# Optimization experiments

Hardware: AMD Instinct MI355X
Metric: run time of the kernel (lower is better)

The kernel has to match this reference:

```python
import jax, jax.numpy as jnp
import numpy as np

F_FEAT = 310   # len(feature_names)
B = 2048       # samples; x has F_FEAT*B elements
H = 32         # sfp_neurons


def _uniform(key, shape, bound):
    return jax.random.uniform(key, shape, jnp.float32, -bound, bound)


def setup_inputs() -> dict:
    key = jax.random.key(0)
    ks = jax.random.split(key, 7)
    x = jax.random.normal(ks[0], (F_FEAT, B), dtype=jnp.float32)
    # Stacked per-feature MLP params (torch Linear default init: U(-1/sqrt(fan_in), +)).
    s1 = 1.0 / np.sqrt(F_FEAT - 1)
    s2 = 1.0 / np.sqrt(H)
    W1 = _uniform(ks[1], (F_FEAT, F_FEAT - 1, H), s1)  # (in, out) layout
    b1 = _uniform(ks[2], (F_FEAT, H), s1)
    W2 = _uniform(ks[3], (F_FEAT, H, H), s2)
    b2 = _uniform(ks[4], (F_FEAT, H), s2)
    W3 = _uniform(ks[5], (F_FEAT, H, H), s2)
    b3 = _uniform(ks[6], (F_FEAT, H), s2)
    return {"x": x, "W1": W1, "b1": b1, "W2": W2, "b2": b2, "W3": W3, "b3": b3}


def reference(x, W1, b1, W2, b2, W3, b3):
    F_, B_ = x.shape
    # Leave-one-out gather: for SFP i, rows [0..i-1, i+1..F-1] of x (feature-major),
    # then the original's view(-1, 1, F-1) reinterprets the flat buffer as (B, F-1).
    idx = jnp.arange(F_ - 1)[None, :]
    idx = idx + (idx >= jnp.arange(F_)[:, None])          # (F, F-1)
    X = x[idx].reshape(F_, B_, F_ - 1)                    # (F, B, F-1) grouped inputs
    h = jax.nn.relu(jnp.einsum('fbk,fkh->fbh', X, W1) + b1[:, None, :])
    h = jax.nn.relu(jnp.einsum('fbh,fhg->fbg', h, W2) + b2[:, None, :])
    h = jax.nn.relu(jnp.einsum('fbh,fhg->fbg', h, W3) + b3[:, None, :])  # (F, B, H)
    # torch.cat of per-SFP .view(-1) == row-major flatten of (F, B, H)
    return h.reshape(-1)
```

## Files before the change

### kernel.cpp

```cpp
#include <hip/hip_runtime.h>

namespace {

constexpr int F_FEAT = 310;
constexpr int KDIM   = 309;
constexpr int BSZ    = 2048;
constexpr int HDIM   = 32;
constexpr int NCH    = 10;
constexpr int NX     = F_FEAT * BSZ;

constexpr int    NBLK8   = NX / 8 + 2;
constexpr size_t CSTR_B  = (size_t)NBLK8 * 16;
constexpr size_t XC_BYTES = CSTR_B * 8;
constexpr size_t W1T_FSTR = 32 * 640;
constexpr size_t W1T_OFF  = XC_BYTES;
constexpr size_t W2T_OFF  = W1T_OFF + (size_t)F_FEAT * W1T_FSTR;
constexpr size_t WT_FSTR  = 2048;
constexpr size_t W3T_OFF  = W2T_OFF + (size_t)F_FEAT * WT_FSTR;
constexpr size_t WS_NEED  = W3T_OFF + (size_t)F_FEAT * WT_FSTR;

typedef __bf16 bf16x8 __attribute__((ext_vector_type(8)));
typedef __bf16 bf16x4 __attribute__((ext_vector_type(4)));
typedef float  f32x4  __attribute__((ext_vector_type(4)));

#define MFMA(a, b, c) __builtin_amdgcn_mfma_f32_16x16x32_bf16((a), (b), (c), 0, 0, 0)

__global__ __launch_bounds__(256) void cvt_x(const float* __restrict__ x,
                                             char* __restrict__ ws) {
    const int m = blockIdx.x * 256 + threadIdx.x;
    const int c = blockIdx.y;
    if (m >= NBLK8) return;
    const int e0 = m * 8 - c;
    bf16x8 v;
    #pragma unroll
    for (int q = 0; q < 8; ++q) {
        const int i = e0 + q;
        const float f = (i >= 0 && i < NX) ? x[i] : 0.f;
        v[q] = (__bf16)f;
    }
    *(bf16x8*)(ws + (size_t)c * CSTR_B + (size_t)m * 16) = v;
}

__global__ __launch_bounds__(256) void cvt_w(const float* __restrict__ W1,
                                             const float* __restrict__ W2,
                                             const float* __restrict__ W3,
                                             char* __restrict__ ws) {
    __shared__ float tile[32][33];
    const int fi = blockIdx.x, tid = threadIdx.x;
    const int kl = tid >> 3;
    const int h4 = (tid & 7) * 4;

    {
        const float* Wg = W1 + (size_t)fi * KDIM * HDIM;
        char* wt = ws + W1T_OFF + (size_t)fi * W1T_FSTR;
        for (int kc = 0; kc < NCH; ++kc) {
            const int k = kc * 32 + kl;
            float4 f = (k < KDIM) ? *(const float4*)&Wg[k * HDIM + h4]
                                  : make_float4(0.f, 0.f, 0.f, 0.f);
            tile[kl][h4 + 0] = f.x; tile[kl][h4 + 1] = f.y;
            tile[kl][h4 + 2] = f.z; tile[kl][h4 + 3] = f.w;
            __syncthreads();
            const int h = kl, kq = h4;
            bf16x4 o;
            #pragma unroll
            for (int j = 0; j < 4; ++j) o[j] = (__bf16)tile[kq + j][h];
            const int boff = (h * 640 + 2 * (kc * 32 + kq)) ^ ((h & 7) << 4);
            *(bf16x4*)(wt + boff) = o;
            __syncthreads();
        }
    }
    {
        const float* Wg = W2 + (size_t)fi * HDIM * HDIM;
        char* wt = ws + W2T_OFF + (size_t)fi * WT_FSTR;
        float4 f = *(const float4*)&Wg[kl * HDIM + h4];
        tile[kl][h4 + 0] = f.x; tile[kl][h4 + 1] = f.y;
        tile[kl][h4 + 2] = f.z; tile[kl][h4 + 3] = f.w;
        __syncthreads();
        bf16x4 o;
        #pragma unroll
        for (int j = 0; j < 4; ++j) o[j] = (__bf16)tile[h4 + j][kl];
        *(bf16x4*)(wt + (kl * 32 + h4) * 2) = o;
        __syncthreads();
    }
    {
        const float* Wg = W3 + (size_t)fi * HDIM * HDIM;
        char* wt = ws + W3T_OFF + (size_t)fi * WT_FSTR;
        float4 f = *(const float4*)&Wg[kl * HDIM + h4];
        tile[kl][h4 + 0] = f.x; tile[kl][h4 + 1] = f.y;
        tile[kl][h4 + 2] = f.z; tile[kl][h4 + 3] = f.w;
        __syncthreads();
        bf16x4 o;
        #pragma unroll
        for (int j = 0; j < 4; ++j) o[j] = (__bf16)tile[h4 + j][kl];
        *(bf16x4*)(wt + (kl * 32 + h4) * 2) = o;
    }
}

template<bool FAST>
__global__ __launch_bounds__(256) void sfp2(
    const float* __restrict__ x,
    const float* __restrict__ W1, const float* __restrict__ b1,
    const float* __restrict__ W2, const float* __restrict__ b2,
    const float* __restrict__ W3, const float* __restrict__ b3,
    const char* __restrict__ ws, float* __restrict__ out)
{
    __shared__ __attribute__((aligned(16))) __bf16 W1s[32 * 320];
    __shared__ __attribute__((aligned(16))) __bf16 h1s[128 * 40];

    int fi, sb;
    if (FAST) {
        const int xc = blockIdx.x & 7, li = blockIdx.x >> 3;
        const int cnt = (xc < 6) ? 39 : 38;
        const int lf = li >> 4;
        if (lf >= cnt) return;
        fi = ((xc < 6) ? xc * 39 : 234 + (xc - 6) * 38) + lf;
        sb = li & 15;
    } else {
        fi = blockIdx.x >> 4; sb = blockIdx.x & 15;
    }

    const int tid = threadIdx.x, lane = tid & 63, wv = tid >> 6;
    const int l15 = lane & 15, l16 = lane >> 4;
    const int lk8 = l16 * 8, r0 = l16 * 4;
    const int b0 = sb << 7, iB = fi << 11;

    if (FAST) {
        const char* src = ws + W1T_OFF + (size_t)fi * W1T_FSTR;
        #pragma unroll
        for (int i = 0; i < 5; ++i) {
            const int off = i * 4096 + tid * 16;
            *(bf16x8*)((char*)W1s + off) = *(const bf16x8*)(src + off);
        }
        __syncthreads();
    }

    const float b1v0 = b1[fi*HDIM + l15], b1v1 = b1[fi*HDIM + 16 + l15];
    const float b2v0 = b2[fi*HDIM + l15], b2v1 = b2[fi*HDIM + 16 + l15];
    const float b3v0 = b3[fi*HDIM + l15], b3v1 = b3[fi*HDIM + 16 + l15];

    auto loadA = [&](int lin) -> bf16x8 {
        if (FAST) {
            if ((unsigned)(iB - 1 - lin) < 7u) {
                bf16x8 r;
                #pragma unroll
                for (int q = 0; q < 8; ++q) {
                    int i = lin + q; i += (i >= iB) ? BSZ : 0;
                    r[q] = *(const __bf16*)(ws + (size_t)i * 2);
                }
                return r;
            }
            const int e  = lin + ((lin >= iB) ? BSZ : 0);
            const int c8 = (-e) & 7;
            return *(const bf16x8*)(ws + (size_t)c8 * CSTR_B + (size_t)(e + c8) * 2);
        } else {
            bf16x8 r;
            #pragma unroll
            for (int q = 0; q < 8; ++q) {
                int i = lin + q; i += (i >= iB) ? BSZ : 0;
                i = (i < NX) ? i : (NX - 1);
                r[q] = (__bf16)x[i];
            }
            return r;
        }
    };

    auto loadW1f = [&](int c, int hrow) -> bf16x8 {
        if (FAST) {
            const int boff = (hrow * 640 + 2 * (c * 32 + lk8)) ^ ((hrow & 7) << 4);
            return *(const bf16x8*)((const char*)W1s + boff);
        } else {
            const float* Wg = W1 + (size_t)fi * KDIM * HDIM;
            bf16x8 r;
            #pragma unroll
            for (int q = 0; q < 8; ++q) {
                const int k = c * 32 + lk8 + q;
                r[q] = (__bf16)((k < KDIM) ? Wg[k * HDIM + hrow] : 0.f);
            }
            return r;
        }
    };

    f32x4 acc00 = {0,0,0,0}, acc01 = {0,0,0,0}, acc10 = {0,0,0,0}, acc11 = {0,0,0,0};
    const int mrow = wv * 32;
    const int lin0 = (b0 + mrow + l15) * KDIM + lk8;
    const int lin1 = lin0 + 16 * KDIM;

    bf16x8 a0 = loadA(lin0),        a1 = loadA(lin1);
    bf16x8 w0 = loadW1f(0, l15),    w1 = loadW1f(0, 16 + l15);
    for (int c = 0; c < NCH; ++c) {
        bf16x8 na0, na1, nw0, nw1;
        if (c + 1 < NCH) {
            na0 = loadA(lin0 + 32 * (c + 1));
            na1 = loadA(lin1 + 32 * (c + 1));
            nw0 = loadW1f(c + 1, l15);
            nw1 = loadW1f(c + 1, 16 + l15);
        }
        acc00 = MFMA(a0, w0, acc00);
        acc01 = MFMA(a0, w1, acc01);
        acc10 = MFMA(a1, w0, acc10);
        acc11 = MFMA(a1, w1, acc11);
        a0 = na0; a1 = na1; w0 = nw0; w1 = nw1;
    }

    constexpr int LDA = 40;
    #pragma unroll
    for (int r = 0; r < 4; ++r) {
        float v;
        v = acc00[r] + b1v0; h1s[(mrow +      r0 + r)*LDA +      l15] = (__bf16)(v > 0.f ? v : 0.f);
        v = acc01[r] + b1v1; h1s[(mrow +      r0 + r)*LDA + 16 + l15] = (__bf16)(v > 0.f ? v : 0.f);
        v = acc10[r] + b1v0; h1s[(mrow + 16 + r0 + r)*LDA +      l15] = (__bf16)(v > 0.f ? v : 0.f);
        v = acc11[r] + b1v1; h1s[(mrow + 16 + r0 + r)*LDA + 16 + l15] = (__bf16)(v > 0.f ? v : 0.f);
    }

    auto loadW23 = [&](const float* Wg, size_t toff, int hrow) -> bf16x8 {
        if (FAST) {
            return *(const bf16x8*)(ws + toff + (size_t)fi * WT_FSTR
                                    + (size_t)(hrow * 32 + lk8) * 2);
        } else {
            bf16x8 r;
            #pragma unroll
            for (int q = 0; q < 8; ++q)
                r[q] = (__bf16)Wg[(size_t)fi * HDIM * HDIM + (lk8 + q) * HDIM + hrow];
            return r;
        }
    };

    const f32x4 z = {0,0,0,0};
    f32x4 c200, c201, c210, c211;
    {
        bf16x8 ha0 = *(const bf16x8*)&h1s[(mrow +      l15)*LDA + lk8];
        bf16x8 ha1 = *(const bf16x8*)&h1s[(mrow + 16 + l15)*LDA + lk8];
        bf16x8 v0 = loadW23(W2, W2T_OFF, l15);
        bf16x8 v1 = loadW23(W2, W2T_OFF, 16 + l15);
        c200 = MFMA(ha0, v0, z); c201 = MFMA(ha0, v1, z);
        c210 = MFMA(ha1, v0, z); c211 = MFMA(ha1, v1, z);
    }
    #pragma unroll
    for (int r = 0; r < 4; ++r) {
        float v;
        v = c200[r] + b2v0; h1s[(mrow +      r0 + r)*LDA +      l15] = (__bf16)(v > 0.f ? v : 0.f);
        v = c201[r] + b2v1; h1s[(mrow +      r0 + r)*LDA + 16 + l15] = (__bf16)(v > 0.f ? v : 0.f);
        v = c210[r] + b2v0; h1s[(mrow + 16 + r0 + r)*LDA +      l15] = (__bf16)(v > 0.f ? v : 0.f);
        v = c211[r] + b2v1; h1s[(mrow + 16 + r0 + r)*LDA + 16 + l15] = (__bf16)(v > 0.f ? v : 0.f);
    }

    f32x4 c300, c301, c310, c311;
    {
        bf16x8 ha0 = *(const bf16x8*)&h1s[(mrow +      l15)*LDA + lk8];
        bf16x8 ha1 = *(const bf16x8*)&h1s[(mrow + 16 + l15)*LDA + lk8];
        bf16x8 v0 = loadW23(W3, W3T_OFF, l15);
        bf16x8 v1 = loadW23(W3, W3T_OFF, 16 + l15);
        c300 = MFMA(ha0, v0, z); c301 = MFMA(ha0, v1, z);
        c310 = MFMA(ha1, v0, z); c311 = MFMA(ha1, v1, z);
    }

    const size_t orow = (size_t)(fi * BSZ + b0 + mrow);
    #pragma unroll
    for (int r = 0; r < 4; ++r) {
        float v;
        v = c300[r] + b3v0; out[(orow +      r0 + r)*HDIM +      l15] = v > 0.f ? v : 0.f;
        v = c301[r] + b3v1; out[(orow +      r0 + r)*HDIM + 16 + l15] = v > 0.f ? v : 0.f;
        v = c310[r] + b3v0; out[(orow + 16 + r0 + r)*HDIM +      l15] = v > 0.f ? v : 0.f;
        v = c311[r] + b3v1; out[(orow + 16 + r0 + r)*HDIM + 16 + l15] = v > 0.f ? v : 0.f;
    }
}

}

extern "C" void kernel_launch(void* const* d_in, const int* in_sizes, int n_in,
                              void* d_out, int out_size, void* d_ws, size_t ws_size,
                              hipStream_t stream) {
    const float* x  = (const float*)d_in[0];
    const float* W1 = (const float*)d_in[1];
    const float* b1 = (const float*)d_in[2];
    const float* W2 = (const float*)d_in[3];
    const float* b2 = (const float*)d_in[4];
    const float* W3 = (const float*)d_in[5];
    const float* b3 = (const float*)d_in[6];
    float* out = (float*)d_out;
    char* ws = (char*)d_ws;

    const bool fast = (ws != nullptr) && (ws_size >= WS_NEED);
    if (fast) {
        hipLaunchKernelGGL(cvt_x, dim3((NBLK8 + 255) / 256, 8), dim3(256), 0, stream, x, ws);
        hipLaunchKernelGGL(cvt_w, dim3(F_FEAT), dim3(256), 0, stream, W1, W2, W3, ws);
        hipLaunchKernelGGL((sfp2<true>), dim3(8 * 39 * 16), dim3(256), 0, stream,
                           x, W1, b1, W2, b2, W3, b3, ws, out);
    } else {
        hipLaunchKernelGGL((sfp2<false>), dim3(F_FEAT * 16), dim3(256), 0, stream,
                           x, W1, b1, W2, b2, W3, b3, ws, out);
    }
}
```

Measured before the change: 77.91 us.

## Merge conversion kernels and read W1 directly from global memory

Result: slower. 99.86 us (+28.2%).

```diff
diff --git a/kernel.cpp b/kernel.cpp
--- a/kernel.cpp
+++ b/kernel.cpp
@@ -9,102 +9,113 @@
 constexpr int NCH    = 10;
 constexpr int NX     = F_FEAT * BSZ;
 
-constexpr int    NBLK8   = NX / 8 + 2;
-constexpr size_t CSTR_B  = (size_t)NBLK8 * 16;
+constexpr int    NBLK8    = NX / 8 + 2;
+constexpr size_t CSTR_B   = (size_t)NBLK8 * 16;
 constexpr size_t XC_BYTES = CSTR_B * 8;
-constexpr size_t W1T_FSTR = 32 * 640;
+constexpr size_t W1T_FSTR = 32 * 320 * 2;
 constexpr size_t W1T_OFF  = XC_BYTES;
 constexpr size_t W2T_OFF  = W1T_OFF + (size_t)F_FEAT * W1T_FSTR;
-constexpr size_t WT_FSTR  = 2048;
+constexpr size_t WT_FSTR  = 32 * 32 * 2;
 constexpr size_t W3T_OFF  = W2T_OFF + (size_t)F_FEAT * WT_FSTR;
 constexpr size_t WS_NEED  = W3T_OFF + (size_t)F_FEAT * WT_FSTR;
 
+constexpr int NBX      = (NBLK8 + 255) / 256;
+constexpr int CVT_XBLK = NBX * 8;
+constexpr int CVT_BLK  = CVT_XBLK + F_FEAT * 6;
+
 typedef __bf16 bf16x8 __attribute__((ext_vector_type(8)));
-typedef __bf16 bf16x4 __attribute__((ext_vector_type(4)));
 typedef float  f32x4  __attribute__((ext_vector_type(4)));
 
 #define MFMA(a, b, c) __builtin_amdgcn_mfma_f32_16x16x32_bf16((a), (b), (c), 0, 0, 0)
 
-__global__ __launch_bounds__(256) void cvt_x(const float* __restrict__ x,
-                                             char* __restrict__ ws) {
-    const int m = blockIdx.x * 256 + threadIdx.x;
-    const int c = blockIdx.y;
-    if (m >= NBLK8) return;
-    const int e0 = m * 8 - c;
-    bf16x8 v;
-    #pragma unroll
-    for (int q = 0; q < 8; ++q) {
-        const int i = e0 + q;
-        const float f = (i >= 0 && i < NX) ? x[i] : 0.f;
-        v[q] = (__bf16)f;
-    }
-    *(bf16x8*)(ws + (size_t)c * CSTR_B + (size_t)m * 16) = v;
-}
-
-__global__ __launch_bounds__(256) void cvt_w(const float* __restrict__ W1,
-                                             const float* __restrict__ W2,
-                                             const float* __restrict__ W3,
-                                             char* __restrict__ ws) {
-    __shared__ float tile[32][33];
-    const int fi = blockIdx.x, tid = threadIdx.x;
-    const int kl = tid >> 3;
-    const int h4 = (tid & 7) * 4;
-
-    {
+__global__ __launch_bounds__(256) void cvt_all(
+    const float* __restrict__ x,  const float* __restrict__ W1,
+    const float* __restrict__ W2, const float* __restrict__ W3,
+    char* __restrict__ ws)
+{
+    __shared__ float tile[64][33];
+    const int b = blockIdx.x, tid = threadIdx.x;
+
+    if (b < CVT_XBLK) {
+        const int c = b / NBX, mb = b - c * NBX;
+        const int m = mb * 256 + tid;
+        if (m >= NBLK8) return;
+        const int e0 = m * 8 - c;
+        bf16x8 v;
+        #pragma unroll
+        for (int q = 0; q < 8; ++q) {
+            const int i = e0 + q;
+            v[q] = (__bf16)((i >= 0 && i < NX) ? x[i] : 0.f);
+        }
+        *(bf16x8*)(ws + (size_t)c * CSTR_B + (size_t)m * 16) = v;
+        return;
+    }
+
+    const int wb = b - CVT_XBLK;
+    const int fi = wb / 6, part = wb - fi * 6;
+
+    if (part < 5) {
         const float* Wg = W1 + (size_t)fi * KDIM * HDIM;
-        char* wt = ws + W1T_OFF + (size_t)fi * W1T_FSTR;
-        for (int kc = 0; kc < NCH; ++kc) {
-            const int k = kc * 32 + kl;
-            float4 f = (k < KDIM) ? *(const float4*)&Wg[k * HDIM + h4]
-                                  : make_float4(0.f, 0.f, 0.f, 0.f);
-            tile[kl][h4 + 0] = f.x; tile[kl][h4 + 1] = f.y;
-            tile[kl][h4 + 2] = f.z; tile[kl][h4 + 3] = f.w;
+        const int row = tid >> 2;
+        const int c8  = (tid & 3) * 8;
+        const int k   = part * 64 + row;
+        float4 f0 = make_float4(0,0,0,0), f1 = f0;
+        if (k < KDIM) {
+            f0 = *(const float4*)&Wg[k * HDIM + c8];
+            f1 = *(const float4*)&Wg[k * HDIM + c8 + 4];
+        }
+        tile[row][c8+0] = f0.x; tile[row][c8+1] = f0.y;
+        tile[row][c8+2] = f0.z; tile[row][c8+3] = f0.w;
+        tile[row][c8+4] = f1.x; tile[row][c8+5] = f1.y;
+        tile[row][c8+6] = f1.z; tile[row][c8+7] = f1.w;
+        __syncthreads();
+        const int h = tid & 31, kq = (tid >> 5) * 8;
+        bf16x8 o;
+        #pragma unroll
+        for (int j = 0; j < 8; ++j) o[j] = (__bf16)tile[kq + j][h];
+        *(bf16x8*)(ws + W1T_OFF + (size_t)fi * W1T_FSTR
+                   + (size_t)(h * 320 + part * 64 + kq) * 2) = o;
+    } else {
+        const int kl = tid >> 3, h4 = (tid & 7) * 4;
+        const int h = tid & 31, kq = (tid >> 5) * 8;
+        {
+            const float* Wg = W2 + (size_t)fi * HDIM * HDIM;
+            float4 f = *(const float4*)&Wg[kl * HDIM + h4];
+            tile[kl][h4+0] = f.x; tile[kl][h4+1] = f.y;
+            tile[kl][h4+2] = f.z; tile[kl][h4+3] = f.w;
             __syncthreads();
-            const int h = kl, kq = h4;
-            bf16x4 o;
-            #pragma unroll
-            for (int j = 0; j < 4; ++j) o[j] = (__bf16)tile[kq + j][h];
-            const int boff = (h * 640 + 2 * (kc * 32 + kq)) ^ ((h & 7) << 4);
-            *(bf16x4*)(wt + boff) = o;
+            if (tid < 128) {
+                bf16x8 o;
+                #pragma unroll
+                for (int j = 0; j < 8; ++j) o[j] = (__bf16)tile[kq + j][h];
+                *(bf16x8*)(ws + W2T_OFF + (size_t)fi * WT_FSTR + (size_t)(h * 32 + kq) * 2) = o;
+            }
             __syncthreads();
         }
-    }
-    {
-        const float* Wg = W2 + (size_t)fi * HDIM * HDIM;
-        char* wt = ws + W2T_OFF + (size_t)fi * WT_FSTR;
-        float4 f = *(const float4*)&Wg[kl * HDIM + h4];
-        tile[kl][h4 + 0] = f.x; tile[kl][h4 + 1] = f.y;
-        tile[kl][h4 + 2] = f.z; tile[kl][h4 + 3] = f.w;
-        __syncthreads();
-        bf16x4 o;
-        #pragma unroll
-        for (int j = 0; j < 4; ++j) o[j] = (__bf16)tile[h4 + j][kl];
-        *(bf16x4*)(wt + (kl * 32 + h4) * 2) = o;
-        __syncthreads();
-    }
-    {
-        const float* Wg = W3 + (size_t)fi * HDIM * HDIM;
-        char* wt = ws + W3T_OFF + (size_t)fi * WT_FSTR;
-        float4 f = *(const float4*)&Wg[kl * HDIM + h4];
-        tile[kl][h4 + 0] = f.x; tile[kl][h4 + 1] = f.y;
-        tile[kl][h4 + 2] = f.z; tile[kl][h4 + 3] = f.w;
-        __syncthreads();
-        bf16x4 o;
-        #pragma unroll
-        for (int j = 0; j < 4; ++j) o[j] = (__bf16)tile[h4 + j][kl];
-        *(bf16x4*)(wt + (kl * 32 + h4) * 2) = o;
+        {
+            const float* Wg = W3 + (size_t)fi * HDIM * HDIM;
+            float4 f = *(const float4*)&Wg[kl * HDIM + h4];
+            tile[kl][h4+0] = f.x; tile[kl][h4+1] = f.y;
+            tile[kl][h4+2] = f.z; tile[kl][h4+3] = f.w;
+            __syncthreads();
+            if (tid < 128) {
+                bf16x8 o;
+                #pragma unroll
+                for (int j = 0; j < 8; ++j) o[j] = (__bf16)tile[kq + j][h];
+                *(bf16x8*)(ws + W3T_OFF + (size_t)fi * WT_FSTR + (size_t)(h * 32 + kq) * 2) = o;
+            }
+        }
     }
 }
 
 template<bool FAST>
-__global__ __launch_bounds__(256) void sfp2(
+__global__ __launch_bounds__(256, 8) void sfp2(
     const float* __restrict__ x,
     const float* __restrict__ W1, const float* __restrict__ b1,
     const float* __restrict__ W2, const float* __restrict__ b2,
     const float* __restrict__ W3, const float* __restrict__ b3,
     const char* __restrict__ ws, float* __restrict__ out)
 {
-    __shared__ __attribute__((aligned(16))) __bf16 W1s[32 * 320];
     __shared__ __attribute__((aligned(16))) __bf16 h1s[128 * 40];
 
     int fi, sb;
@@ -124,16 +135,6 @@
     const int lk8 = l16 * 8, r0 = l16 * 4;
     const int b0 = sb << 7, iB = fi << 11;
 
-    if (FAST) {
-        const char* src = ws + W1T_OFF + (size_t)fi * W1T_FSTR;
-        #pragma unroll
-        for (int i = 0; i < 5; ++i) {
-            const int off = i * 4096 + tid * 16;
-            *(bf16x8*)((char*)W1s + off) = *(const bf16x8*)(src + off);
-        }
-        __syncthreads();
-    }
-
     const float b1v0 = b1[fi*HDIM + l15], b1v1 = b1[fi*HDIM + 16 + l15];
     const float b2v0 = b2[fi*HDIM + l15], b2v1 = b2[fi*HDIM + 16 + l15];
     const float b3v0 = b3[fi*HDIM + l15], b3v1 = b3[fi*HDIM + 16 + l15];
@@ -166,8 +167,8 @@
 
     auto loadW1f = [&](int c, int hrow) -> bf16x8 {
         if (FAST) {
-            const int boff = (hrow * 640 + 2 * (c * 32 + lk8)) ^ ((hrow & 7) << 4);
-            return *(const bf16x8*)((const char*)W1s + boff);
+            return *(const bf16x8*)(ws + W1T_OFF + (size_t)fi * W1T_FSTR
+                                    + (size_t)(hrow * 320 + c * 32 + lk8) * 2);
         } else {
             const float* Wg = W1 + (size_t)fi * KDIM * HDIM;
             bf16x8 r;
@@ -185,8 +186,8 @@
     const int lin0 = (b0 + mrow + l15) * KDIM + lk8;
     const int lin1 = lin0 + 16 * KDIM;
 
-    bf16x8 a0 = loadA(lin0),        a1 = loadA(lin1);
-    bf16x8 w0 = loadW1f(0, l15),    w1 = loadW1f(0, 16 + l15);
+    bf16x8 a0 = loadA(lin0),     a1 = loadA(lin1);
+    bf16x8 w0 = loadW1f(0, l15), w1 = loadW1f(0, 16 + l15);
     for (int c = 0; c < NCH; ++c) {
         bf16x8 na0, na1, nw0, nw1;
         if (c + 1 < NCH) {
@@ -282,8 +283,7 @@
 
     const bool fast = (ws != nullptr) && (ws_size >= WS_NEED);
     if (fast) {
-        hipLaunchKernelGGL(cvt_x, dim3((NBLK8 + 255) / 256, 8), dim3(256), 0, stream, x, ws);
-        hipLaunchKernelGGL(cvt_w, dim3(F_FEAT), dim3(256), 0, stream, W1, W2, W3, ws);
+        hipLaunchKernelGGL(cvt_all, dim3(CVT_BLK), dim3(256), 0, stream, x, W1, W2, W3, ws);
         hipLaunchKernelGGL((sfp2<true>), dim3(8 * 39 * 16), dim3(256), 0, stream,
                            x, W1, b1, W2, b2, W3, b3, ws, out);
     } else {
```
